# Optimization experiments

Hardware: AMD Instinct MI355X
Metric: run time of the kernel (lower is better)

Reference implementation:

```python
import jax, jax.numpy as jnp
import numpy as np

H = 16          # n_heads
DH = 128        # head_dim
DR = 64         # rope_dim
DC = DH - DR    # content_dim = 64
THETA = 10000.0
SCALE = 1.0 / np.sqrt(DH)


def _rope_tables(T, dtype):
    inv = 1.0 / (THETA ** (jnp.arange(0, DR, 2, dtype=jnp.float32) / DR))  # [DR/2]
    t = jnp.arange(T, dtype=jnp.float32)
    freqs = jnp.outer(t, inv)  # [T, DR/2]
    return jnp.cos(freqs).astype(dtype), jnp.sin(freqs).astype(dtype)


def _apply_rope(x, cos, sin):
    # x: [B,H,T,DR]; cos/sin: [T,DR/2] broadcast over B,H
    d = x.shape[-1] // 2
    x1, x2 = x[..., :d], x[..., d:]
    return jnp.concatenate([x1 * cos - x2 * sin, x1 * sin + x2 * cos], axis=-1)


def setup_inputs() -> dict:
    key = jax.random.key(0)
    ks = jax.random.split(key, 9)
    B, T, D = 1, 2048, 2048
    s = 0.02
    return {
        "x": jax.random.normal(ks[0], (B, T, D), jnp.float32),
        "Wq_down": jax.random.normal(ks[1], (D, 512), jnp.float32) * s,
        "Wq_up": jax.random.normal(ks[2], (512, H * DC), jnp.float32) * s,
        "Wq_rope": jax.random.normal(ks[3], (D, H * DR), jnp.float32) * s,
        "Wkv_down": jax.random.normal(ks[4], (D, 512), jnp.float32) * s,
        "Wk_up": jax.random.normal(ks[5], (512, H * DC), jnp.float32) * s,
        "Wv_up": jax.random.normal(ks[6], (512, H * DH), jnp.float32) * s,
        "Wk_rope": jax.random.normal(ks[7], (D, H * DR), jnp.float32) * s,
        "Wo": jax.random.normal(ks[8], (H * DH, D), jnp.float32) * s,
    }


def reference(x, Wq_down, Wq_up, Wq_rope, Wkv_down, Wk_up, Wv_up, Wk_rope, Wo):
    B, T, D = x.shape
    # low-rank query path: down then up, content part only
    q_content = ((x @ Wq_down) @ Wq_up).reshape(B, T, H, DC).transpose(0, 2, 1, 3)
    q_pos = (x @ Wq_rope).reshape(B, T, H, DR).transpose(0, 2, 1, 3)
    kv_latent = x @ Wkv_down                    # [B,T,d_latent]
    k_pos = (x @ Wk_rope).reshape(B, T, H, DR).transpose(0, 2, 1, 3)

    cos, sin = _rope_tables(T, x.dtype)
    q_pos = _apply_rope(q_pos, cos, sin)
    k_pos = _apply_rope(k_pos, cos, sin)

    k_content = (kv_latent @ Wk_up).reshape(B, T, H, DC).transpose(0, 2, 1, 3)
    v = (kv_latent @ Wv_up).reshape(B, T, H, DH).transpose(0, 2, 1, 3)

    q = jnp.concatenate([q_content, q_pos], axis=-1)  # [B,H,T,DH]
    k = jnp.concatenate([k_content, k_pos], axis=-1)  # [B,H,T,DH]

    scores = jnp.einsum("bhtd,bhsd->bhts", q, k) * SCALE
    causal = jnp.tril(jnp.ones((T, T), dtype=bool))
    scores = jnp.where(causal, scores, jnp.finfo(scores.dtype).min)
    attn = jax.nn.softmax(scores, axis=-1)
    out = jnp.einsum("bhts,bhsd->bhtd", attn, v)       # [B,H,T,DH]
    out = out.transpose(0, 2, 1, 3).reshape(B, T, H * DH)
    return out @ Wo
```

## Files before the change

### kernel.cpp

```cpp
#include <hip/hip_runtime.h>
#include <math.h>

#define T_SEQ 2048
#define D_MODEL 2048
#define H_HEADS 16
#define DH 128
#define DR 64
#define DC 64
#define D_LAT 512
#define NSPLIT 3
#define QSCALE (0.08838834764831845f * 1.4426950408889634f)

typedef __attribute__((ext_vector_type(8))) short short8;
typedef __attribute__((ext_vector_type(4))) short short4v;
typedef __attribute__((ext_vector_type(4))) float f32x4;

#if __has_builtin(__builtin_amdgcn_exp2f)
#define EXP2(x) __builtin_amdgcn_exp2f(x)
#else
#define EXP2(x) exp2f(x)
#endif

__device__ __forceinline__ float bf2f(short b) {
    unsigned u = ((unsigned)(unsigned short)b) << 16;
    return __builtin_bit_cast(float, u);
}
__device__ __forceinline__ short f2bf(float f) {
    unsigned u = __builtin_bit_cast(unsigned, f);
    unsigned r = u + 0x7fffu + ((u >> 16) & 1u);
    return (short)(r >> 16);
}
__device__ __forceinline__ short f2bf_trunc(float f) {
    return (short)(__builtin_bit_cast(unsigned, f) >> 16);
}

#define GLD_LDS(gp, lp) \
    __builtin_amdgcn_global_load_lds( \
        (const __attribute__((address_space(1))) void*)(gp), \
        (__attribute__((address_space(3))) void*)(lp), 16, 0, 0)

__device__ __forceinline__ void ct_tile(float (*tile)[33],
                                        const float* __restrict__ W,
                                        short* __restrict__ Wt,
                                        int R, int C, int ldo, int rel) {
    int bx = rel % (C / 32), by = rel / (C / 32);
    int c0 = bx * 32, r0 = by * 32;
    int tx = threadIdx.x & 31, ty = threadIdx.x >> 5;
    #pragma unroll
    for (int i = 0; i < 4; ++i)
        tile[ty + i * 8][tx] = W[(size_t)(r0 + ty + i * 8) * C + c0 + tx];
    __syncthreads();
    #pragma unroll
    for (int i = 0; i < 4; ++i)
        Wt[(size_t)(c0 + ty + i * 8) * ldo + r0 + tx] = f2bf(tile[tx][ty + i * 8]);
    __syncthreads();
}

__global__ __launch_bounds__(256) void prep(const float* __restrict__ x,
                                            short* __restrict__ xb,
                                            const float* __restrict__ Wqd,
                                            const float* __restrict__ Wkvd,
                                            const float* __restrict__ Wqr,
                                            const float* __restrict__ Wkr,
                                            const float* __restrict__ Wqu,
                                            const float* __restrict__ Wku,
                                            const float* __restrict__ Wvu,
                                            const float* __restrict__ Wo,
                                            short* __restrict__ WdT,
                                            short* __restrict__ WupT2,
                                            short* __restrict__ WoT) {
    __shared__ float tile[32][33];
    int bid = blockIdx.x;
    if (bid < 4096) {
        int i = bid * 1024 + threadIdx.x * 4;
        float4 f = *(const float4*)&x[i];
        short4v o;
        o.x = f2bf(f.x); o.y = f2bf(f.y); o.z = f2bf(f.z); o.w = f2bf(f.w);
        *(short4v*)&xb[i] = o;
    } else if (bid < 5120) {
        ct_tile(tile, Wqd,  WdT + (size_t)0 * 2048,    2048, 512,  2048, bid - 4096);
    } else if (bid < 6144) {
        ct_tile(tile, Wkvd, WdT + (size_t)512 * 2048,  2048, 512,  2048, bid - 5120);
    } else if (bid < 8192) {
        ct_tile(tile, Wqr,  WdT + (size_t)1024 * 2048, 2048, 1024, 2048, bid - 6144);
    } else if (bid < 10240) {
        ct_tile(tile, Wkr,  WdT + (size_t)2048 * 2048, 2048, 1024, 2048, bid - 8192);
    } else if (bid < 10752) {
        ct_tile(tile, Wqu,  WupT2 + (size_t)0 * 512,    512, 1024, 512, bid - 10240);
    } else if (bid < 11264) {
        ct_tile(tile, Wku,  WupT2 + (size_t)1024 * 512, 512, 1024, 512, bid - 10752);
    } else if (bid < 12288) {
        ct_tile(tile, Wvu,  WupT2 + (size_t)2048 * 512, 512, 2048, 512, bid - 11264);
    } else {
        ct_tile(tile, Wo,   WoT, 2048, 2048, 2048, bid - 12288);
    }
}

__global__ __launch_bounds__(256) void transpose_bf16(const short* __restrict__ in,
                                                      short* __restrict__ outb,
                                                      int ldi) {
    __shared__ short tile[64][65];
    int c0 = blockIdx.x * 64, t0 = blockIdx.y * 64;
    int tx = threadIdx.x & 31, ty = threadIdx.x >> 5;
    #pragma unroll
    for (int i = 0; i < 8; ++i) {
        int r = ty + i * 8;
        int vv = *(const int*)&in[(size_t)(t0 + r) * ldi + c0 + tx * 2];
        tile[r][tx * 2]     = (short)(vv & 0xffff);
        tile[r][tx * 2 + 1] = (short)(((unsigned)vv) >> 16);
    }
    __syncthreads();
    #pragma unroll
    for (int i = 0; i < 8; ++i) {
        int c = ty + i * 8;
        unsigned lo = (unsigned short)tile[tx * 2][c];
        unsigned hi = (unsigned short)tile[tx * 2 + 1][c];
        *(int*)&outb[(size_t)(c0 + c) * 2048 + t0 + tx * 2] = (int)(lo | (hi << 16));
    }
}

__global__ __launch_bounds__(256) void gemm_bt(const short* __restrict__ A,
                                               const short* __restrict__ A2,
                                               const short* __restrict__ Bt,
                                               short* __restrict__ C0,
                                               short* __restrict__ C1,
                                               short* __restrict__ C2,
                                               short* __restrict__ C3,
                                               int N, int Kblk,
                                               int lda, int ldb, int ldc,
                                               int ncut, int scut, float cscale) {
    __shared__ short As[128 * 32];
    __shared__ short Bs[128 * 32];
    const int tid = threadIdx.x;
    const int wave = tid >> 6, lane = tid & 63;
    const int lin = blockIdx.x;
    const int X = N >> 7, Xq = X >> 2;
    const int xcd = lin & 7;
    int r = lin >> 3;
    const int bx = (xcd & 3) * Xq + (r % Xq); r /= Xq;
    const int by = (xcd >> 2) * 8 + (r & 7);
    const int bz = r >> 3;
    const int row0 = by * 128, col0 = bx * 128;
    const int kbase = bz * Kblk;
    const short* Ause = (col0 < ncut) ? A : A2;
    short* Cuse = (bz == 0) ? C0 : (bz == 1) ? C1 : (bz == 2) ? C2 : C3;
    const int wr = (wave >> 1) * 64, wc = (wave & 1) * 64;
    const int lr = lane & 15, quad = lane >> 4;

    f32x4 acc[4][4];
    #pragma unroll
    for (int i = 0; i < 4; ++i)
        #pragma unroll
        for (int j = 0; j < 4; ++j) acc[i][j] = (f32x4){0.f, 0.f, 0.f, 0.f};

    for (int k0 = kbase; k0 < kbase + Kblk; k0 += 32) {
        __syncthreads();
        #pragma unroll
        for (int it = 0; it < 2; ++it) {
            int idx = wave * 64 + it * 256 + lane;
            const short* ga = Ause + (size_t)(row0 + (idx >> 2)) * lda + k0 + (idx & 3) * 8;
            const short* gb = Bt   + (size_t)(col0 + (idx >> 2)) * ldb + k0 + (idx & 3) * 8;
            int lds0 = (wave * 64 + it * 256) * 8;
            GLD_LDS(ga, &As[lds0]);
            GLD_LDS(gb, &Bs[lds0]);
        }
        __syncthreads();

        short8 af[4], bfr[4];
        #pragma unroll
        for (int i = 0; i < 4; ++i)
            af[i] = *(const short8*)&As[(wr + i * 16 + lr) * 32 + quad * 8];
        #pragma unroll
        for (int j = 0; j < 4; ++j)
            bfr[j] = *(const short8*)&Bs[(wc + j * 16 + lr) * 32 + quad * 8];
        #pragma unroll
        for (int i = 0; i < 4; ++i)
            #pragma unroll
            for (int j = 0; j < 4; ++j)
                acc[i][j] = __builtin_amdgcn_mfma_f32_16x16x32_bf16(af[i], bfr[j],
                                                                   acc[i][j], 0, 0, 0);
    }

    const float sc = (col0 < scut) ? cscale : 1.0f;
    #pragma unroll
    for (int i = 0; i < 4; ++i) {
        int rb = row0 + wr + i * 16 + quad * 4;
        #pragma unroll
        for (int j = 0; j < 4; ++j) {
            int c = col0 + wc + j * 16 + lr;
            #pragma unroll
            for (int rr = 0; rr < 4; ++rr)
                Cuse[(size_t)(rb + rr) * ldc + c] = f2bf(acc[i][j][rr] * sc);
        }
    }
}

__global__ __launch_bounds__(192) void finish_down(short* __restrict__ cat,
                                                   const short* __restrict__ pdown) {
    const int t = blockIdx.x;
    const int k8 = threadIdx.x * 8;
    const int c0 = ((k8 >> 5) << 6) + (k8 & 31);
    const size_t lo = (size_t)t * 3072 + c0;
    const size_t hi = lo + 32;
    short8 al = *(const short8*)&cat[lo];
    short8 ah = *(const short8*)&cat[hi];
    short8 bl = *(const short8*)&pdown[lo];
    short8 bh = *(const short8*)&pdown[hi];
    float xl[8], xh[8];
    #pragma unroll
    for (int j = 0; j < 8; ++j) {
        xl[j] = bf2f(al[j]) + bf2f(bl[j]);
        xh[j] = bf2f(ah[j]) + bf2f(bh[j]);
    }
    if (c0 >= 1024) {
        float sc = (c0 < 2048) ? QSCALE : 1.0f;
        #pragma unroll
        for (int j = 0; j < 8; ++j) {
            int i = (c0 & 31) + j;
            float freq = (float)t * __powf(10000.0f, -(float)i / 32.0f);
            float cs = __cosf(freq), sn = __sinf(freq);
            float r1 = (xl[j] * cs - xh[j] * sn) * sc;
            float r2 = (xl[j] * sn + xh[j] * cs) * sc;
            xl[j] = r1; xh[j] = r2;
        }
    }
    short8 ol, oh;
    #pragma unroll
    for (int j = 0; j < 8; ++j) { ol[j] = f2bf(xl[j]); oh[j] = f2bf(xh[j]); }
    *(short8*)&cat[lo] = ol;
    *(short8*)&cat[hi] = oh;
}

__global__ __launch_bounds__(256) void add_out_f32(const short* __restrict__ p0,
                                                   const short* __restrict__ p1,
                                                   const short* __restrict__ p2,
                                                   const short* __restrict__ p3,
                                                   float* __restrict__ out) {
    int i = (blockIdx.x * 256 + threadIdx.x) * 4;
    short4v a = *(const short4v*)&p0[i];
    short4v b = *(const short4v*)&p1[i];
    short4v c = *(const short4v*)&p2[i];
    short4v d = *(const short4v*)&p3[i];
    float4 o;
    o.x = (bf2f(a.x) + bf2f(b.x)) + (bf2f(c.x) + bf2f(d.x));
    o.y = (bf2f(a.y) + bf2f(b.y)) + (bf2f(c.y) + bf2f(d.y));
    o.z = (bf2f(a.z) + bf2f(b.z)) + (bf2f(c.z) + bf2f(d.z));
    o.w = (bf2f(a.w) + bf2f(b.w)) + (bf2f(c.w) + bf2f(d.w));
    *(float4*)&out[i] = o;
}

__global__ __launch_bounds__(256) void attn_mla_split(const short* __restrict__ qkup,
                                                      const short* __restrict__ cat,
                                                      const short* __restrict__ vT,
                                                      short* __restrict__ Opart01,
                                                      short* __restrict__ Opart2,
                                                      float* __restrict__ lpart) {
    const int lin = blockIdx.x;
    const int xcd = lin & 7;
    int r_ = lin >> 3;
    const int h = xcd + 8 * (r_ & 1);
    r_ >>= 1;
    const int qt2 = 15 - (r_ & 15);
    const int g = r_ >> 4;
    const int tid = threadIdx.x;
    const int wave = tid >> 6, lane = tid & 63;
    const int lr = lane & 15, quad = lane >> 4;

    __shared__ short Ks[32 * 128];
    __shared__ short Vst[128 * 32];
    __shared__ short Ps[4][2][16 * 40];

    short* Og = (g < 2) ? Opart01 + (size_t)g * (T_SEQ * 2048) : Opart2;
    const short8 ones = {0x3F80, 0x3F80, 0x3F80, 0x3F80,
                         0x3F80, 0x3F80, 0x3F80, 0x3F80};

    const int Q0 = qt2 * 128;
    const int qrowA = Q0 + wave * 16;
    const int qrowB = qrowA + 64;
    const int nchunk = 4 * qt2 + 4;

    short8 qf[2][4];
    #pragma unroll
    for (int sb = 0; sb < 2; ++sb) {
        int t = (sb ? qrowB : qrowA) + lr;
        #pragma unroll
        for (int kci = 0; kci < 4; ++kci) {
            const short* src = (kci < 2)
                ? qkup + (size_t)t * 4096 + h * 64
                : cat + (size_t)t * 3072 + 1024 + h * 64;
            qf[sb][kci] = *(const short8*)&src[(kci & 1) * 32 + quad * 8];
        }
    }

    const int idx = wave * 64 + lane;
    const int key = idx >> 4;
    const int cg = (idx & 15) ^ (key & 15);
    const short* kp0 = (cg < 8)
        ? qkup + (size_t)key * 4096 + 1024 + h * 64 + cg * 8
        : cat + (size_t)key * 3072 + 2048 + h * 64 + (cg - 8) * 8;
    const int kst = (cg < 8) ? 4096 : 3072;
    const short* kp1 = kp0 + (size_t)16 * kst;
    const int dd = idx >> 2;
    const int scg = (idx & 3) ^ (dd & 3);
    const short* vp0 = vT + (size_t)(h * 128 + dd) * 2048 + scg * 8;
    const short* vp1 = vp0 + (size_t)64 * 2048;
    kp0 += (size_t)g * 32 * kst; kp1 += (size_t)g * 32 * kst;
    vp0 += g * 32;               vp1 += g * 32;
    const int kadv = NSPLIT * 32 * kst;
    const int vadv = NSPLIT * 32;
    const int ldsA = (wave * 64) * 8;
    const int ldsB = (wave * 64 + 256) * 8;

    f32x4 Oacc[2][8];
    #pragma unroll
    for (int sb = 0; sb < 2; ++sb)
        #pragma unroll
        for (int d = 0; d < 8; ++d) Oacc[sb][d] = (f32x4){0.f, 0.f, 0.f, 0.f};
    f32x4 Lacc[2];
    Lacc[0] = (f32x4){0.f, 0.f, 0.f, 0.f};
    Lacc[1] = (f32x4){0.f, 0.f, 0.f, 0.f};

    for (int c = g; c < nchunk; c += NSPLIT) {
        const int s0 = c * 32;
        __syncthreads();
        GLD_LDS(kp0, &Ks[ldsA]);
        GLD_LDS(kp1, &Ks[ldsB]);
        GLD_LDS(vp0, &Vst[ldsA]);
        GLD_LDS(vp1, &Vst[ldsB]);
        kp0 += kadv; kp1 += kadv; vp0 += vadv; vp1 += vadv;
        __syncthreads();
        if (s0 > qrowB + 15) continue;
        const bool actA = (s0 <= qrowA + 15);

        f32x4 sacc[2][2];
        #pragma unroll
        for (int sb = 0; sb < 2; ++sb)
            #pragma unroll
            for (int n = 0; n < 2; ++n) sacc[sb][n] = (f32x4){0.f, 0.f, 0.f, 0.f};
        #pragma unroll
        for (int n = 0; n < 2; ++n) {
            #pragma unroll
            for (int kci = 0; kci < 4; ++kci) {
                short8 kf = *(const short8*)
                    &Ks[(n * 16 + lr) * 128 + ((kci * 4 + quad) ^ lr) * 8];
                if (actA)
                    sacc[0][n] = __builtin_amdgcn_mfma_f32_16x16x32_bf16(
                        qf[0][kci], kf, sacc[0][n], 0, 0, 0);
                sacc[1][n] = __builtin_amdgcn_mfma_f32_16x16x32_bf16(
                    qf[1][kci], kf, sacc[1][n], 0, 0, 0);
            }
        }
        #pragma unroll
        for (int sb = 0; sb < 2; ++sb) {
            if (sb == 0 && !actA) continue;
            const int qrow0 = sb ? qrowB : qrowA;
            if (s0 + 31 > qrow0) {
                #pragma unroll
                for (int r = 0; r < 4; ++r) {
                    int qg = qrow0 + quad * 4 + r;
                    #pragma unroll
                    for (int n = 0; n < 2; ++n) {
                        int s = s0 + n * 16 + lr;
                        sacc[sb][n][r] = (s <= qg) ? sacc[sb][n][r] : -1e30f;
                    }
                }
            }
            #pragma unroll
            for (int r = 0; r < 4; ++r) {
                Ps[wave][sb][(quad * 4 + r) * 40 + lr] =
                    f2bf_trunc(EXP2(sacc[sb][0][r]));
                Ps[wave][sb][(quad * 4 + r) * 40 + 16 + lr] =
                    f2bf_trunc(EXP2(sacc[sb][1][r]));
            }
        }
        short8 pfA, pfB;
        if (actA) {
            pfA = *(const short8*)&Ps[wave][0][lr * 40 + quad * 8];
            Lacc[0] = __builtin_amdgcn_mfma_f32_16x16x32_bf16(pfA, ones,
                                                              Lacc[0], 0, 0, 0);
        }
        pfB = *(const short8*)&Ps[wave][1][lr * 40 + quad * 8];
        Lacc[1] = __builtin_amdgcn_mfma_f32_16x16x32_bf16(pfB, ones,
                                                          Lacc[1], 0, 0, 0);
        #pragma unroll
        for (int dt = 0; dt < 8; ++dt) {
            short8 vf = *(const short8*)
                &Vst[(dt * 16 + lr) * 32 + (quad ^ (lr & 3)) * 8];
            if (actA)
                Oacc[0][dt] = __builtin_amdgcn_mfma_f32_16x16x32_bf16(
                    pfA, vf, Oacc[0][dt], 0, 0, 0);
            Oacc[1][dt] = __builtin_amdgcn_mfma_f32_16x16x32_bf16(
                pfB, vf, Oacc[1][dt], 0, 0, 0);
        }
    }

    #pragma unroll
    for (int sb = 0; sb < 2; ++sb) {
        const int qrow0 = sb ? qrowB : qrowA;
        #pragma unroll
        for (int r = 0; r < 4; ++r) {
            int t = qrow0 + quad * 4 + r;
            #pragma unroll
            for (int dt = 0; dt < 8; ++dt)
                Og[(size_t)t * 2048 + h * 128 + dt * 16 + lr] =
                    f2bf(Oacc[sb][dt][r]);
        }
        if (lr == 0) {
            #pragma unroll
            for (int r = 0; r < 4; ++r) {
                int t = qrow0 + quad * 4 + r;
                lpart[(size_t)(g * T_SEQ + t) * H_HEADS + h] = Lacc[sb][r];
            }
        }
    }
}

__global__ __launch_bounds__(256) void attn_combine(const short* __restrict__ O01,
                                                    const short* __restrict__ O2,
                                                    const float* __restrict__ lpart,
                                                    short* __restrict__ ao) {
    const int t = blockIdx.x;
    const int h = threadIdx.x >> 4;
    const int di = (threadIdx.x & 15) * 8;
    size_t off = (size_t)t * 2048 + h * 128 + di;
    short8 a = *(const short8*)&O01[off];
    short8 b = *(const short8*)&O01[(size_t)T_SEQ * 2048 + off];
    short8 c = *(const short8*)&O2[off];
    float den = lpart[(size_t)(0 * T_SEQ + t) * H_HEADS + h] +
                lpart[(size_t)(1 * T_SEQ + t) * H_HEADS + h] +
                lpart[(size_t)(2 * T_SEQ + t) * H_HEADS + h];
    float inv = 1.0f / den;
    short8 o;
    #pragma unroll
    for (int j = 0; j < 8; ++j)
        o[j] = f2bf((bf2f(a[j]) + bf2f(b[j]) + bf2f(c[j])) * inv);
    *(short8*)&ao[off] = o;
}

extern "C" void kernel_launch(void* const* d_in, const int* in_sizes, int n_in,
                              void* d_out, int out_size, void* d_ws, size_t ws_size,
                              hipStream_t stream) {
    const float* x        = (const float*)d_in[0];
    const float* Wq_down  = (const float*)d_in[1];
    const float* Wq_up    = (const float*)d_in[2];
    const float* Wq_rope  = (const float*)d_in[3];
    const float* Wkv_down = (const float*)d_in[4];
    const float* Wk_up    = (const float*)d_in[5];
    const float* Wv_up    = (const float*)d_in[6];
    const float* Wk_rope  = (const float*)d_in[7];
    const float* Wo       = (const float*)d_in[8];
    float* out = (float*)d_out;

    short* p = (short*)d_ws;
    short* xb     = p; p += (size_t)2048 * 2048;
    short* WoT    = p; p += (size_t)2048 * 2048;
    short* cat    = p; p += (size_t)2048 * 3072;
    short* upcat2 = p; p += (size_t)2048 * 4096;
    short* WdT    = p; p += (size_t)3072 * 2048;
    short* WupT2  = p; p += (size_t)4096 * 512;
    short* vT     = p; p += (size_t)2048 * 2048;
    float* lpart  = (float*)p;
    short* pdown   = upcat2;
    short* aob     = cat;
    short* Opart01 = WdT;
    short* Opart2  = xb;
    short* pw0     = upcat2;
    short* pw1     = upcat2 + (size_t)2048 * 2048;
    short* pw2     = WdT;
    short* pw3     = WdT + (size_t)2048 * 2048;

    prep<<<dim3(16384), 256, 0, stream>>>(x, xb, Wq_down, Wkv_down, Wq_rope,
                                          Wk_rope, Wq_up, Wk_up, Wv_up, Wo,
                                          WdT, WupT2, WoT);

    gemm_bt<<<dim3(24 * 16 * 2), 256, 0, stream>>>(xb, xb, WdT, cat, pdown,
                                                   nullptr, nullptr,
                                                   3072, 1024,
                                                   2048, 2048, 3072, 1 << 30, 0, 1.f);

    finish_down<<<dim3(2048), 192, 0, stream>>>(cat, pdown);

    gemm_bt<<<dim3(32 * 16 * 1), 256, 0, stream>>>(cat, cat + 512, WupT2,
                                                   upcat2, nullptr, nullptr, nullptr,
                                                   4096, 512,
                                                   3072, 512, 4096, 1024, 1024, QSCALE);

    transpose_bf16<<<dim3(32, 32), 256, 0, stream>>>(upcat2 + 2048, vT, 4096);

    attn_mla_split<<<dim3(16 * 16 * NSPLIT), 256, 0, stream>>>(upcat2, cat, vT,
                                                               Opart01, Opart2, lpart);
    attn_combine<<<dim3(2048), 256, 0, stream>>>(Opart01, Opart2, lpart, aob);

    gemm_bt<<<dim3(16 * 16 * 4), 256, 0, stream>>>(aob, aob, WoT, pw0, pw1, pw2, pw3,
                                                   2048, 512,
                                                   2048, 2048, 2048, 1 << 30, 0, 1.f);
    add_out_f32<<<dim3(2048 * 2048 / 1024), 256, 0, stream>>>(pw0, pw1, pw2, pw3, out);
}
```

Baseline: 282.6 us.

## Double-buffer K/V LDS tiles in split attention and raise MFMA wave priority

The attention kernel now keeps two LDS buffers for K and V. It issues the global-to-LDS loads for the next chunk before computing on the current one, and waits on vmcnt plus a barrier only at the end of each iteration. This is meant to hide global load latency behind the QK and PV MFMA work and to cut one of the two barriers per chunk. It also wraps the MFMA sections in s_setprio to favour the compute waves. The cost is double the K/V LDS footprint, which may reduce occupancy, and there is a possible WAR hazard on Ps because no barrier sits between iterations.

```diff
diff --git a/kernel.cpp b/kernel.cpp
--- a/kernel.cpp
+++ b/kernel.cpp
@@ -266,8 +266,8 @@
     const int wave = tid >> 6, lane = tid & 63;
     const int lr = lane & 15, quad = lane >> 4;
 
-    __shared__ short Ks[32 * 128];
-    __shared__ short Vst[128 * 32];
+    __shared__ short Ks[2][32 * 128];
+    __shared__ short Vst[2][128 * 32];
     __shared__ short Ps[4][2][16 * 40];
 
     short* Og = (g < 2) ? Opart01 + (size_t)g * (T_SEQ * 2048) : Opart2;
@@ -320,78 +320,102 @@
     Lacc[0] = (f32x4){0.f, 0.f, 0.f, 0.f};
     Lacc[1] = (f32x4){0.f, 0.f, 0.f, 0.f};
 
+    GLD_LDS(kp0, &Ks[0][ldsA]);
+    GLD_LDS(kp1, &Ks[0][ldsB]);
+    GLD_LDS(vp0, &Vst[0][ldsA]);
+    GLD_LDS(vp1, &Vst[0][ldsB]);
+    kp0 += kadv; kp1 += kadv; vp0 += vadv; vp1 += vadv;
+    asm volatile("s_waitcnt vmcnt(0)" ::: "memory");
+    __builtin_amdgcn_s_barrier();
+
+    int cur = 0;
     for (int c = g; c < nchunk; c += NSPLIT) {
         const int s0 = c * 32;
-        __syncthreads();
-        GLD_LDS(kp0, &Ks[ldsA]);
-        GLD_LDS(kp1, &Ks[ldsB]);
-        GLD_LDS(vp0, &Vst[ldsA]);
-        GLD_LDS(vp1, &Vst[ldsB]);
-        kp0 += kadv; kp1 += kadv; vp0 += vadv; vp1 += vadv;
-        __syncthreads();
-        if (s0 > qrowB + 15) continue;
-        const bool actA = (s0 <= qrowA + 15);
-
-        f32x4 sacc[2][2];
-        #pragma unroll
-        for (int sb = 0; sb < 2; ++sb)
-            #pragma unroll
-            for (int n = 0; n < 2; ++n) sacc[sb][n] = (f32x4){0.f, 0.f, 0.f, 0.f};
-        #pragma unroll
-        for (int n = 0; n < 2; ++n) {
-            #pragma unroll
-            for (int kci = 0; kci < 4; ++kci) {
-                short8 kf = *(const short8*)
-                    &Ks[(n * 16 + lr) * 128 + ((kci * 4 + quad) ^ lr) * 8];
-                if (actA)
-                    sacc[0][n] = __builtin_amdgcn_mfma_f32_16x16x32_bf16(
-                        qf[0][kci], kf, sacc[0][n], 0, 0, 0);
-                sacc[1][n] = __builtin_amdgcn_mfma_f32_16x16x32_bf16(
-                    qf[1][kci], kf, sacc[1][n], 0, 0, 0);
+        const bool havenext = (c + NSPLIT < nchunk);
+        if (havenext) {
+            GLD_LDS(kp0, &Ks[cur ^ 1][ldsA]);
+            GLD_LDS(kp1, &Ks[cur ^ 1][ldsB]);
+            GLD_LDS(vp0, &Vst[cur ^ 1][ldsA]);
+            GLD_LDS(vp1, &Vst[cur ^ 1][ldsB]);
+            kp0 += kadv; kp1 += kadv; vp0 += vadv; vp1 += vadv;
+        }
+
+        if (s0 <= qrowB + 15) {
+            const bool actA = (s0 <= qrowA + 15);
+            const short* Kc = Ks[cur];
+            const short* Vc = Vst[cur];
+
+            f32x4 sacc[2][2];
+            #pragma unroll
+            for (int sb = 0; sb < 2; ++sb)
+                #pragma unroll
+                for (int n = 0; n < 2; ++n) sacc[sb][n] = (f32x4){0.f, 0.f, 0.f, 0.f};
+            __builtin_amdgcn_s_setprio(1);
+            #pragma unroll
+            for (int n = 0; n < 2; ++n) {
+                #pragma unroll
+                for (int kci = 0; kci < 4; ++kci) {
+                    short8 kf = *(const short8*)
+                        &Kc[(n * 16 + lr) * 128 + ((kci * 4 + quad) ^ lr) * 8];
+                    if (actA)
+                        sacc[0][n] = __builtin_amdgcn_mfma_f32_16x16x32_bf16(
+                            qf[0][kci], kf, sacc[0][n], 0, 0, 0);
+                    sacc[1][n] = __builtin_amdgcn_mfma_f32_16x16x32_bf16(
+                        qf[1][kci], kf, sacc[1][n], 0, 0, 0);
+                }
             }
-        }
-        #pragma unroll
-        for (int sb = 0; sb < 2; ++sb) {
-            if (sb == 0 && !actA) continue;
-            const int qrow0 = sb ? qrowB : qrowA;
-            if (s0 + 31 > qrow0) {
+            __builtin_amdgcn_s_setprio(0);
+            #pragma unroll
+            for (int sb = 0; sb < 2; ++sb) {
+                if (sb == 0 && !actA) continue;
+                const int qrow0 = sb ? qrowB : qrowA;
+                if (s0 + 31 > qrow0) {
+                    #pragma unroll
+                    for (int r = 0; r < 4; ++r) {
+                        int qg = qrow0 + quad * 4 + r;
+                        #pragma unroll
+                        for (int n = 0; n < 2; ++n) {
+                            int s = s0 + n * 16 + lr;
+                            sacc[sb][n][r] = (s <= qg) ? sacc[sb][n][r] : -1e30f;
+                        }
+                    }
+                }
                 #pragma unroll
                 for (int r = 0; r < 4; ++r) {
-                    int qg = qrow0 + quad * 4 + r;
-                    #pragma unroll
-                    for (int n = 0; n < 2; ++n) {
-                        int s = s0 + n * 16 + lr;
-                        sacc[sb][n][r] = (s <= qg) ? sacc[sb][n][r] : -1e30f;
-                    }
+                    Ps[wave][sb][(quad * 4 + r) * 40 + lr] =
+                        f2bf_trunc(EXP2(sacc[sb][0][r]));
+                    Ps[wave][sb][(quad * 4 + r) * 40 + 16 + lr] =
+                        f2bf_trunc(EXP2(sacc[sb][1][r]));
                 }
             }
-            #pragma unroll
-            for (int r = 0; r < 4; ++r) {
-                Ps[wave][sb][(quad * 4 + r) * 40 + lr] =
-                    f2bf_trunc(EXP2(sacc[sb][0][r]));
-                Ps[wave][sb][(quad * 4 + r) * 40 + 16 + lr] =
-                    f2bf_trunc(EXP2(sacc[sb][1][r]));
+            short8 pfA, pfB;
+            __builtin_amdgcn_s_setprio(1);
+            if (actA) {
+                pfA = *(const short8*)&Ps[wave][0][lr * 40 + quad * 8];
+                Lacc[0] = __builtin_amdgcn_mfma_f32_16x16x32_bf16(pfA, ones,
+                                                                  Lacc[0], 0, 0, 0);
             }
-        }
-        short8 pfA, pfB;
-        if (actA) {
-            pfA = *(const short8*)&Ps[wave][0][lr * 40 + quad * 8];
-            Lacc[0] = __builtin_amdgcn_mfma_f32_16x16x32_bf16(pfA, ones,
-                                                              Lacc[0], 0, 0, 0);
-        }
-        pfB = *(const short8*)&Ps[wave][1][lr * 40 + quad * 8];
-        Lacc[1] = __builtin_amdgcn_mfma_f32_16x16x32_bf16(pfB, ones,
-                                                          Lacc[1], 0, 0, 0);
-        #pragma unroll
-        for (int dt = 0; dt < 8; ++dt) {
-            short8 vf = *(const short8*)
-                &Vst[(dt * 16 + lr) * 32 + (quad ^ (lr & 3)) * 8];
-            if (actA)
-                Oacc[0][dt] = __builtin_amdgcn_mfma_f32_16x16x32_bf16(
-                    pfA, vf, Oacc[0][dt], 0, 0, 0);
-            Oacc[1][dt] = __builtin_amdgcn_mfma_f32_16x16x32_bf16(
-                pfB, vf, Oacc[1][dt], 0, 0, 0);
-        }
+            pfB = *(const short8*)&Ps[wave][1][lr * 40 + quad * 8];
+            Lacc[1] = __builtin_amdgcn_mfma_f32_16x16x32_bf16(pfB, ones,
+                                                              Lacc[1], 0, 0, 0);
+            #pragma unroll
+            for (int dt = 0; dt < 8; ++dt) {
+                short8 vf = *(const short8*)
+                    &Vc[(dt * 16 + lr) * 32 + (quad ^ (lr & 3)) * 8];
+                if (actA)
+                    Oacc[0][dt] = __builtin_amdgcn_mfma_f32_16x16x32_bf16(
+                        pfA, vf, Oacc[0][dt], 0, 0, 0);
+                Oacc[1][dt] = __builtin_amdgcn_mfma_f32_16x16x32_bf16(
+                    pfB, vf, Oacc[1][dt], 0, 0, 0);
+            }
+            __builtin_amdgcn_s_setprio(0);
+        }
+
+        if (havenext) {
+            asm volatile("s_waitcnt vmcnt(0)" ::: "memory");
+            __builtin_amdgcn_s_barrier();
+        }
+        cur ^= 1;
     }
 
     #pragma unroll
```

Result: no change. 285.4 us (+1.0%).

## Replace fixed 3-way KV split with balanced contiguous segments per query tile

Applied to the files above, without the earlier changes.

The causal attention work was split into three strided KV groups for every query tile, so blocks for short tiles did little work and blocks for long tiles did a lot. The new code gives each query tile a variable number of contiguous KV segments of at most 14 chunks, 46 segments per head, for 736 blocks with roughly equal work each. Partial outputs and denominators go to per-segment slots, and the combine kernel loops over however many segments each tile has. The cost is a more complex slot mapping and a variable-length reduction loop in the combine step. It also relies on the slots fitting in the reused workspace slabs.

```diff
diff --git a/kernel.cpp b/kernel.cpp
--- a/kernel.cpp
+++ b/kernel.cpp
@@ -8,7 +8,8 @@
 #define DR 64
 #define DC 64
 #define D_LAT 512
-#define NSPLIT 3
+#define SEGLEN 14
+#define NSEG_TOT 46
 #define QSCALE (0.08838834764831845f * 1.4426950408889634f)
 
 typedef __attribute__((ext_vector_type(8))) short short8;
@@ -252,16 +253,27 @@
 __global__ __launch_bounds__(256) void attn_mla_split(const short* __restrict__ qkup,
                                                       const short* __restrict__ cat,
                                                       const short* __restrict__ vT,
-                                                      short* __restrict__ Opart01,
-                                                      short* __restrict__ Opart2,
+                                                      short* __restrict__ slabA,
+                                                      short* __restrict__ slabB,
                                                       float* __restrict__ lpart) {
     const int lin = blockIdx.x;
     const int xcd = lin & 7;
-    int r_ = lin >> 3;
-    const int h = xcd + 8 * (r_ & 1);
-    r_ >>= 1;
-    const int qt2 = 15 - (r_ & 15);
-    const int g = r_ >> 4;
+    int k_ = lin >> 3;
+    const int h = xcd + 8 * (k_ & 1);
+    const int pp = k_ >> 1;
+    int qt = 0, s = 0, acc = 0;
+    #pragma unroll
+    for (int q = 0; q < 16; ++q) {
+        const int ns = (4 * q + 4 + SEGLEN - 1) / SEGLEN;
+        if (pp >= acc) { qt = q; s = pp - acc; }
+        acc += ns;
+    }
+    const int nchunk = 4 * qt + 4;
+    const int nsq = (nchunk + SEGLEN - 1) / SEGLEN;
+    const int cbase = nchunk / nsq, crem = nchunk % nsq;
+    const int c0 = s * cbase + (s < crem ? s : crem);
+    const int c1 = c0 + cbase + (s < crem ? 1 : 0);
+
     const int tid = threadIdx.x;
     const int wave = tid >> 6, lane = tid & 63;
     const int lr = lane & 15, quad = lane >> 4;
@@ -270,14 +282,12 @@
     __shared__ short Vst[128 * 32];
     __shared__ short Ps[4][2][16 * 40];
 
-    short* Og = (g < 2) ? Opart01 + (size_t)g * (T_SEQ * 2048) : Opart2;
     const short8 ones = {0x3F80, 0x3F80, 0x3F80, 0x3F80,
                          0x3F80, 0x3F80, 0x3F80, 0x3F80};
 
-    const int Q0 = qt2 * 128;
+    const int Q0 = qt * 128;
     const int qrowA = Q0 + wave * 16;
     const int qrowB = qrowA + 64;
-    const int nchunk = 4 * qt2 + 4;
 
     short8 qf[2][4];
     #pragma unroll
@@ -304,10 +314,10 @@
     const int scg = (idx & 3) ^ (dd & 3);
     const short* vp0 = vT + (size_t)(h * 128 + dd) * 2048 + scg * 8;
     const short* vp1 = vp0 + (size_t)64 * 2048;
-    kp0 += (size_t)g * 32 * kst; kp1 += (size_t)g * 32 * kst;
-    vp0 += g * 32;               vp1 += g * 32;
-    const int kadv = NSPLIT * 32 * kst;
-    const int vadv = NSPLIT * 32;
+    kp0 += (size_t)c0 * 32 * kst; kp1 += (size_t)c0 * 32 * kst;
+    vp0 += c0 * 32;               vp1 += c0 * 32;
+    const int kadv = 32 * kst;
+    const int vadv = 32;
     const int ldsA = (wave * 64) * 8;
     const int ldsB = (wave * 64 + 256) * 8;
 
@@ -320,7 +330,7 @@
     Lacc[0] = (f32x4){0.f, 0.f, 0.f, 0.f};
     Lacc[1] = (f32x4){0.f, 0.f, 0.f, 0.f};
 
-    for (int c = g; c < nchunk; c += NSPLIT) {
+    for (int c = c0; c < c1; ++c) {
         const int s0 = c * 32;
         __syncthreads();
         GLD_LDS(kp0, &Ks[ldsA]);
@@ -360,8 +370,8 @@
                     int qg = qrow0 + quad * 4 + r;
                     #pragma unroll
                     for (int n = 0; n < 2; ++n) {
-                        int s = s0 + n * 16 + lr;
-                        sacc[sb][n][r] = (s <= qg) ? sacc[sb][n][r] : -1e30f;
+                        int sidx = s0 + n * 16 + lr;
+                        sacc[sb][n][r] = (sidx <= qg) ? sacc[sb][n][r] : -1e30f;
                     }
                 }
             }
@@ -394,47 +404,55 @@
         }
     }
 
+    const int slot = h * NSEG_TOT + pp;
+    short* slotp = (slot < 512) ? slabA + (size_t)slot * 16384
+                                : slabB + (size_t)(slot - 512) * 16384;
     #pragma unroll
     for (int sb = 0; sb < 2; ++sb) {
-        const int qrow0 = sb ? qrowB : qrowA;
+        const int rbase = wave * 16 + sb * 64 + quad * 4;
         #pragma unroll
         for (int r = 0; r < 4; ++r) {
-            int t = qrow0 + quad * 4 + r;
             #pragma unroll
             for (int dt = 0; dt < 8; ++dt)
-                Og[(size_t)t * 2048 + h * 128 + dt * 16 + lr] =
-                    f2bf(Oacc[sb][dt][r]);
+                slotp[(rbase + r) * 128 + dt * 16 + lr] = f2bf(Oacc[sb][dt][r]);
         }
         if (lr == 0) {
             #pragma unroll
-            for (int r = 0; r < 4; ++r) {
-                int t = qrow0 + quad * 4 + r;
-                lpart[(size_t)(g * T_SEQ + t) * H_HEADS + h] = Lacc[sb][r];
-            }
-        }
-    }
-}
-
-__global__ __launch_bounds__(256) void attn_combine(const short* __restrict__ O01,
-                                                    const short* __restrict__ O2,
+            for (int r = 0; r < 4; ++r)
+                lpart[(size_t)slot * 128 + rbase + r] = Lacc[sb][r];
+        }
+    }
+}
+
+__global__ __launch_bounds__(256) void attn_combine(const short* __restrict__ slabA,
+                                                    const short* __restrict__ slabB,
                                                     const float* __restrict__ lpart,
                                                     short* __restrict__ ao) {
     const int t = blockIdx.x;
+    const int qt = t >> 7, rl = t & 127;
     const int h = threadIdx.x >> 4;
     const int di = (threadIdx.x & 15) * 8;
-    size_t off = (size_t)t * 2048 + h * 128 + di;
-    short8 a = *(const short8*)&O01[off];
-    short8 b = *(const short8*)&O01[(size_t)T_SEQ * 2048 + off];
-    short8 c = *(const short8*)&O2[off];
-    float den = lpart[(size_t)(0 * T_SEQ + t) * H_HEADS + h] +
-                lpart[(size_t)(1 * T_SEQ + t) * H_HEADS + h] +
-                lpart[(size_t)(2 * T_SEQ + t) * H_HEADS + h];
+    int pf = 0;
+    #pragma unroll
+    for (int q = 0; q < 16; ++q)
+        if (q < qt) pf += (4 * q + 4 + SEGLEN - 1) / SEGLEN;
+    const int ns = (4 * qt + 4 + SEGLEN - 1) / SEGLEN;
+    float o[8] = {0.f, 0.f, 0.f, 0.f, 0.f, 0.f, 0.f, 0.f};
+    float den = 0.f;
+    for (int s = 0; s < ns; ++s) {
+        const int slot = h * NSEG_TOT + pf + s;
+        const short* sp = (slot < 512) ? slabA + (size_t)slot * 16384
+                                       : slabB + (size_t)(slot - 512) * 16384;
+        short8 v = *(const short8*)&sp[rl * 128 + di];
+        #pragma unroll
+        for (int j = 0; j < 8; ++j) o[j] += bf2f(v[j]);
+        den += lpart[(size_t)slot * 128 + rl];
+    }
     float inv = 1.0f / den;
-    short8 o;
-    #pragma unroll
-    for (int j = 0; j < 8; ++j)
-        o[j] = f2bf((bf2f(a[j]) + bf2f(b[j]) + bf2f(c[j])) * inv);
-    *(short8*)&ao[off] = o;
+    short8 ov;
+    #pragma unroll
+    for (int j = 0; j < 8; ++j) ov[j] = f2bf(o[j] * inv);
+    *(short8*)&ao[(size_t)t * 2048 + h * 128 + di] = ov;
 }
 
 extern "C" void kernel_launch(void* const* d_in, const int* in_sizes, int n_in,
@@ -462,8 +480,8 @@
     float* lpart  = (float*)p;
     short* pdown   = upcat2;
     short* aob     = cat;
-    short* Opart01 = WdT;
-    short* Opart2  = xb;
+    short* slabA   = WdT;
+    short* slabB   = xb;
     short* pw0     = upcat2;
     short* pw1     = upcat2 + (size_t)2048 * 2048;
     short* pw2     = WdT;
@@ -487,9 +505,9 @@
 
     transpose_bf16<<<dim3(32, 32), 256, 0, stream>>>(upcat2 + 2048, vT, 4096);
 
-    attn_mla_split<<<dim3(16 * 16 * NSPLIT), 256, 0, stream>>>(upcat2, cat, vT,
-                                                               Opart01, Opart2, lpart);
-    attn_combine<<<dim3(2048), 256, 0, stream>>>(Opart01, Opart2, lpart, aob);
+    attn_mla_split<<<dim3(16 * NSEG_TOT), 256, 0, stream>>>(upcat2, cat, vT,
+                                                            slabA, slabB, lpart);
+    attn_combine<<<dim3(2048), 256, 0, stream>>>(slabA, slabB, lpart, aob);
 
     gemm_bt<<<dim3(16 * 16 * 4), 256, 0, stream>>>(aob, aob, WoT, pw0, pw1, pw2, pw3,
                                                    2048, 512,
```

New measurement: 287.5 us. No clear change (+1.8%).
